# Kernel optimization log

Measured on AMD Instinct MI355X. Metric: run time of the kernel, lower is better.

Reference implementation:

```python
import jax, jax.numpy as jnp
import numpy as np

B, D, P, K, L_S = 512, 1024, 64, 16, 16


def _make_M():
    # fixed signed mask: top-left PxP block = -1, bottom-left KxP block = +1
    M = np.zeros((P + K, P + K), dtype=np.float32)
    M[:P, :P] = -1.0
    M[P:, :P] = +1.0
    return jnp.asarray(M)


def setup_inputs() -> dict:
    key = jax.random.key(0)
    k1, k2, k3 = jax.random.split(key, 3)
    X_tilde = jax.random.normal(k1, (B, D, P + K), dtype=jnp.float32)
    y_train = jax.random.normal(k2, (B, P), dtype=jnp.float32)
    gamma = jax.random.normal(k3, (D,), dtype=jnp.float32) * 0.01
    return {"X_tilde": X_tilde, "y_train": y_train, "gamma": gamma}


def reference(X_tilde, y_train, gamma):
    M = _make_M()  # [P+K, P+K]
    Bsz = X_tilde.shape[0]
    # h0 = [y_train, 0_K]  -> [B, P+K]
    h0 = jnp.concatenate([y_train, jnp.zeros((Bsz, K), dtype=y_train.dtype)], axis=-1)
    # score[b,m,n] = sum_d gamma[d] * X[b,d,m] * X[b,d,n] / P
    weighted = gamma[None, :, None] * X_tilde  # [B, D, P+K]
    score = jnp.einsum('bdm,bdn->bmn', weighted, X_tilde) / float(P)
    masked_score = M[None, :, :] * score  # [B, P+K, P+K]
    inv_L = 1.0 / float(L_S)

    def step(h, _):
        h = h + inv_L * jnp.einsum('bmn,bn->bm', masked_score, h)
        return h, None

    h, _ = jax.lax.scan(step, h0, None, length=L_S)
    return h[:, P:]
```

## Files before the change

### kernel.cpp

```cpp
#include <hip/hip_runtime.h>


namespace {
typedef __attribute__((ext_vector_type(8))) short bf16x8;
typedef __attribute__((ext_vector_type(4))) float f32x4;
typedef __attribute__((ext_vector_type(4))) float fv4;
typedef __attribute__((ext_vector_type(2))) unsigned uv2;

constexpr int kB  = 512;
constexpr int kD  = 1024;
constexpr int kP  = 64;
constexpr int kKK = 16;
constexpr int kLS = 16;
constexpr int kThreads = 640;
constexpr int kKc = 64;
constexpr int kNC = kD / kKc;

constexpr int TB    = 4096;
constexpr int ASZ   = 80 * 64 * 2;
constexpr int BSZ   = 64 * 64 * 2;
constexpr int BUFSZ = ASZ + BSZ;
constexpr int LDS_BYTES = TB + 2 * BUFSZ;

__device__ __forceinline__ unsigned short bf16_bits(float x) {
  unsigned u = __builtin_bit_cast(unsigned, x);
  u += 0x7fffu + ((u >> 16) & 1u);
  return (unsigned short)(u >> 16);
}
__device__ __forceinline__ unsigned bpack(float lo, float hi) {
  return (unsigned)bf16_bits(lo) | ((unsigned)bf16_bits(hi) << 16);
}

__global__ void __launch_bounds__(kThreads)
tcsf_kernel(const float* __restrict__ X, const float* __restrict__ y,
            const float* __restrict__ gamma, float* __restrict__ out) {
  __shared__ __align__(16) char smem[LDS_BYTES];
  float* gs = reinterpret_cast<float*>(smem);

  const int t = threadIdx.x;
  const int b = blockIdx.x;
  const int l = t & 63;
  const int w = t >> 6;
  const int grp = (w >= 5) ? 1 : 0;
  const int slab = grp ? (w - 5) : w;
  const int tg = grp ? (t - 320) : t;
  const int ct = tg % 20;
  const int kt = tg / 20;

  for (int i = t; i < kD; i += kThreads) gs[i] = gamma[i];

  const fv4* Xg = reinterpret_cast<const fv4*>(X) + (size_t)b * (kD * 80 / 4);

  f32x4 acc[4];
#pragma unroll
  for (int nt = 0; nt < 4; ++nt) acc[nt] = (f32x4)(0.f);

  fv4 v0, v1, v2, v3;

  const int rA   = 16 * slab + (l & 15);
  const int cb   = grp * 64 + (l >> 4) * 16;
  const int fswz = (l & 7) << 4;

  {
    const int c0 = grp;
    const int base = (c0 * kKc + 4 * kt) * 20 + ct;
    v0 = Xg[base]; v1 = Xg[base + 20]; v2 = Xg[base + 40]; v3 = Xg[base + 60];
  }
  __syncthreads();
  if (grp == 0) {
    char* Ab = smem + TB;
    char* Bb = Ab + ASZ;
    const fv4 g4 = *reinterpret_cast<const fv4*>(gs + 4 * kt);
#pragma unroll
    for (int j = 0; j < 4; ++j) {
      const int m = 4 * ct + j;
      const int rowo = m * 128;
      const int col = (8 * kt) ^ ((m & 7) << 4);
      uv2 wa; wa.x = bpack(v0[j], v1[j]); wa.y = bpack(v2[j], v3[j]);
      *reinterpret_cast<uv2*>(Ab + rowo + col) = wa;
      if (ct < 16) {
        uv2 wb; wb.x = bpack(g4[0] * v0[j], g4[1] * v1[j]);
        wb.y = bpack(g4[2] * v2[j], g4[3] * v3[j]);
        *reinterpret_cast<uv2*>(Bb + rowo + col) = wb;
      }
    }
  }
  __syncthreads();

  for (int c = 0; c < kNC; ++c) {
    const int pl = c & 1;
    if (c + 2 < kNC && grp == pl) {
      const int base = ((c + 2) * kKc + 4 * kt) * 20 + ct;
      v0 = Xg[base]; v1 = Xg[base + 20]; v2 = Xg[base + 40]; v3 = Xg[base + 60];
    }
    if (c + 1 < kNC && grp != pl) {
      char* Ab = smem + TB + ((c + 1) & 1) * BUFSZ;
      char* Bb = Ab + ASZ;
      const fv4 g4 = *reinterpret_cast<const fv4*>(gs + (c + 1) * kKc + 4 * kt);
#pragma unroll
      for (int j = 0; j < 4; ++j) {
        const int m = 4 * ct + j;
        const int rowo = m * 128;
        const int col = (8 * kt) ^ ((m & 7) << 4);
        uv2 wa; wa.x = bpack(v0[j], v1[j]); wa.y = bpack(v2[j], v3[j]);
        *reinterpret_cast<uv2*>(Ab + rowo + col) = wa;
        if (ct < 16) {
          uv2 wb; wb.x = bpack(g4[0] * v0[j], g4[1] * v1[j]);
          wb.y = bpack(g4[2] * v2[j], g4[3] * v3[j]);
          *reinterpret_cast<uv2*>(Bb + rowo + col) = wb;
        }
      }
    }
    {
      const char* Ab = smem + TB + pl * BUFSZ;
      const char* Bb = Ab + ASZ;
      const bf16x8 a = *reinterpret_cast<const bf16x8*>(Ab + rA * 128 + (cb ^ fswz));
#pragma unroll
      for (int nt = 0; nt < 4; ++nt) {
        const bf16x8 bb = *reinterpret_cast<const bf16x8*>(
            Bb + (16 * nt + (l & 15)) * 128 + (cb ^ fswz));
        acc[nt] = __builtin_amdgcn_mfma_f32_16x16x32_bf16(a, bb, acc[nt], 0, 0, 0);
      }
    }
    __syncthreads();
  }

  float* Gl = reinterpret_cast<float*>(smem + TB);
  float* hp = Gl + 80 * 65;
  constexpr float invP = 1.0f / 64.0f;
  if (grp) {
#pragma unroll
    for (int nt = 0; nt < 4; ++nt)
#pragma unroll
      for (int r = 0; r < 4; ++r)
        Gl[(16 * slab + (l >> 4) * 4 + r) * 65 + 16 * nt + (l & 15)] = acc[nt][r];
  }
  __syncthreads();
  if (!grp) {
#pragma unroll
    for (int nt = 0; nt < 4; ++nt)
#pragma unroll
      for (int r = 0; r < 4; ++r) {
        const int idx = (16 * slab + (l >> 4) * 4 + r) * 65 + 16 * nt + (l & 15);
        Gl[idx] = (Gl[idx] + acc[nt][r]) * invP;
      }
  }
  if (t < kP) hp[t] = y[b * kP + t];
  __syncthreads();

  const int m = t >> 3;
  const int part = t & 7;
  const float* Grow = Gl + m * 65 + part * 8;
  float hk = 0.f;
  constexpr float invL = 1.0f / kLS;
  for (int s = 0; s < kLS; ++s) {
    const float* hpc = hp + (s & 1) * kP;
    const float* hpp = hpc + part * 8;
    float d0 = 0.f, d1 = 0.f, d2 = 0.f, d3 = 0.f;
#pragma unroll
    for (int i = 0; i < 8; i += 4) {
      d0 = fmaf(Grow[i + 0], hpp[i + 0], d0);
      d1 = fmaf(Grow[i + 1], hpp[i + 1], d1);
      d2 = fmaf(Grow[i + 2], hpp[i + 2], d2);
      d3 = fmaf(Grow[i + 3], hpp[i + 3], d3);
    }
    float dot = (d0 + d1) + (d2 + d3);
    dot += __shfl_xor(dot, 1);
    dot += __shfl_xor(dot, 2);
    dot += __shfl_xor(dot, 4);
    if (part == 0) {
      if (m < kP) hp[((s + 1) & 1) * kP + m] = hpc[m] - invL * dot;
      else        hk += invL * dot;
    }
    __syncthreads();
  }
  if (part == 0 && m >= kP) out[b * kKK + (m - kP)] = hk;
}

}

extern "C" void kernel_launch(void* const* d_in, const int* in_sizes, int n_in,
                              void* d_out, int out_size, void* d_ws, size_t ws_size,
                              hipStream_t stream) {
  const float* X     = (const float*)d_in[0];
  const float* y     = (const float*)d_in[1];
  const float* gamma = (const float*)d_in[2];
  float* out = (float*)d_out;
  tcsf_kernel<<<dim3(kB), dim3(kThreads), 0, stream>>>(X, y, gamma, out);
}
```

Baseline: 41.30 us.

## Reorder prefetch after staging, change LDS swizzle, hoist offsets and y load

Each group now stages its register-held chunk into LDS first and then issues the global loads for chunk c+3, rather than loading before staging. This makes the loaded registers free earlier and gives the loads a full iteration to arrive. The XOR swizzle now also mixes row bits 2-4 to cut LDS bank conflicts between writes and reads. MFMA fragment offsets are hoisted out of the loop, and the y load is issued at kernel start to hide its latency. The cost is a slightly more complex swizzle computation.

```diff
diff --git a/kernel.cpp b/kernel.cpp
--- a/kernel.cpp
+++ b/kernel.cpp
@@ -17,8 +17,8 @@
 constexpr int kNC = kD / kKc;
 
 constexpr int TB    = 4096;
-constexpr int ASZ   = 80 * 64 * 2;
-constexpr int BSZ   = 64 * 64 * 2;
+constexpr int ASZ   = 80 * 128;
+constexpr int BSZ   = 64 * 128;
 constexpr int BUFSZ = ASZ + BSZ;
 constexpr int LDS_BYTES = TB + 2 * BUFSZ;
 
@@ -29,6 +29,28 @@
 }
 __device__ __forceinline__ unsigned bpack(float lo, float hi) {
   return (unsigned)bf16_bits(lo) | ((unsigned)bf16_bits(hi) << 16);
+}
+__device__ __forceinline__ int fswz(int r) {
+  return ((r & 7) ^ ((r >> 2) & 7)) << 4;
+}
+
+__device__ __forceinline__ void stage_chunk(char* __restrict__ Ab, char* __restrict__ Bb,
+                                            int ct, int kt,
+                                            const fv4& v0, const fv4& v1,
+                                            const fv4& v2, const fv4& v3,
+                                            const fv4& g4) {
+#pragma unroll
+  for (int j = 0; j < 4; ++j) {
+    const int m = 4 * ct + j;
+    const int off = m * 128 + ((8 * kt) ^ fswz(m));
+    uv2 wa; wa.x = bpack(v0[j], v1[j]); wa.y = bpack(v2[j], v3[j]);
+    *reinterpret_cast<uv2*>(Ab + off) = wa;
+    if (ct < 16) {
+      uv2 wb; wb.x = bpack(g4[0] * v0[j], g4[1] * v1[j]);
+      wb.y = bpack(g4[2] * v2[j], g4[3] * v3[j]);
+      *reinterpret_cast<uv2*>(Bb + off) = wb;
+    }
+  }
 }
 
 __global__ void __launch_bounds__(kThreads)
@@ -47,6 +69,8 @@
   const int ct = tg % 20;
   const int kt = tg / 20;
 
+  float yv = 0.f;
+  if (t < kP) yv = y[b * kP + t];
   for (int i = t; i < kD; i += kThreads) gs[i] = gamma[i];
 
   const fv4* Xg = reinterpret_cast<const fv4*>(X) + (size_t)b * (kD * 80 / 4);
@@ -57,70 +81,48 @@
 
   fv4 v0, v1, v2, v3;
 
-  const int rA   = 16 * slab + (l & 15);
-  const int cb   = grp * 64 + (l >> 4) * 16;
-  const int fswz = (l & 7) << 4;
-
   {
-    const int c0 = grp;
-    const int base = (c0 * kKc + 4 * kt) * 20 + ct;
+    const int base = (grp * kKc + 4 * kt) * 20 + ct;
     v0 = Xg[base]; v1 = Xg[base + 20]; v2 = Xg[base + 40]; v3 = Xg[base + 60];
   }
   __syncthreads();
-  if (grp == 0) {
-    char* Ab = smem + TB;
-    char* Bb = Ab + ASZ;
+  if (!grp) {
     const fv4 g4 = *reinterpret_cast<const fv4*>(gs + 4 * kt);
-#pragma unroll
-    for (int j = 0; j < 4; ++j) {
-      const int m = 4 * ct + j;
-      const int rowo = m * 128;
-      const int col = (8 * kt) ^ ((m & 7) << 4);
-      uv2 wa; wa.x = bpack(v0[j], v1[j]); wa.y = bpack(v2[j], v3[j]);
-      *reinterpret_cast<uv2*>(Ab + rowo + col) = wa;
-      if (ct < 16) {
-        uv2 wb; wb.x = bpack(g4[0] * v0[j], g4[1] * v1[j]);
-        wb.y = bpack(g4[2] * v2[j], g4[3] * v3[j]);
-        *reinterpret_cast<uv2*>(Bb + rowo + col) = wb;
-      }
-    }
+    stage_chunk(smem + TB, smem + TB + ASZ, ct, kt, v0, v1, v2, v3, g4);
+    const int base = (2 * kKc + 4 * kt) * 20 + ct;
+    v0 = Xg[base]; v1 = Xg[base + 20]; v2 = Xg[base + 40]; v3 = Xg[base + 60];
   }
   __syncthreads();
 
+  const int rA = 16 * slab + (l & 15);
+  const int cbb = grp * 64 + (l >> 4) * 16;
+  const int offA = rA * 128 + (cbb ^ fswz(rA));
+  int offB[4];
+#pragma unroll
+  for (int nt = 0; nt < 4; ++nt) {
+    const int rB = 16 * nt + (l & 15);
+    offB[nt] = rB * 128 + (cbb ^ fswz(rB));
+  }
+
   for (int c = 0; c < kNC; ++c) {
-    const int pl = c & 1;
-    if (c + 2 < kNC && grp == pl) {
-      const int base = ((c + 2) * kKc + 4 * kt) * 20 + ct;
-      v0 = Xg[base]; v1 = Xg[base + 20]; v2 = Xg[base + 40]; v3 = Xg[base + 60];
-    }
-    if (c + 1 < kNC && grp != pl) {
-      char* Ab = smem + TB + ((c + 1) & 1) * BUFSZ;
-      char* Bb = Ab + ASZ;
-      const fv4 g4 = *reinterpret_cast<const fv4*>(gs + (c + 1) * kKc + 4 * kt);
-#pragma unroll
-      for (int j = 0; j < 4; ++j) {
-        const int m = 4 * ct + j;
-        const int rowo = m * 128;
-        const int col = (8 * kt) ^ ((m & 7) << 4);
-        uv2 wa; wa.x = bpack(v0[j], v1[j]); wa.y = bpack(v2[j], v3[j]);
-        *reinterpret_cast<uv2*>(Ab + rowo + col) = wa;
-        if (ct < 16) {
-          uv2 wb; wb.x = bpack(g4[0] * v0[j], g4[1] * v1[j]);
-          wb.y = bpack(g4[2] * v2[j], g4[3] * v3[j]);
-          *reinterpret_cast<uv2*>(Bb + rowo + col) = wb;
-        }
+    if (grp == ((c + 1) & 1)) {
+      if (c + 1 < kNC) {
+        const fv4 g4 = *reinterpret_cast<const fv4*>(gs + (c + 1) * kKc + 4 * kt);
+        char* Ab = smem + TB + ((c + 1) & 1) * BUFSZ;
+        stage_chunk(Ab, Ab + ASZ, ct, kt, v0, v1, v2, v3, g4);
+      }
+      if (c + 3 < kNC) {
+        const int base = ((c + 3) * kKc + 4 * kt) * 20 + ct;
+        v0 = Xg[base]; v1 = Xg[base + 20]; v2 = Xg[base + 40]; v3 = Xg[base + 60];
       }
     }
-    {
-      const char* Ab = smem + TB + pl * BUFSZ;
-      const char* Bb = Ab + ASZ;
-      const bf16x8 a = *reinterpret_cast<const bf16x8*>(Ab + rA * 128 + (cb ^ fswz));
+    const char* Ab = smem + TB + (c & 1) * BUFSZ;
+    const char* Bb = Ab + ASZ;
+    const bf16x8 a = *reinterpret_cast<const bf16x8*>(Ab + offA);
 #pragma unroll
-      for (int nt = 0; nt < 4; ++nt) {
-        const bf16x8 bb = *reinterpret_cast<const bf16x8*>(
-            Bb + (16 * nt + (l & 15)) * 128 + (cb ^ fswz));
-        acc[nt] = __builtin_amdgcn_mfma_f32_16x16x32_bf16(a, bb, acc[nt], 0, 0, 0);
-      }
+    for (int nt = 0; nt < 4; ++nt) {
+      const bf16x8 bb = *reinterpret_cast<const bf16x8*>(Bb + offB[nt]);
+      acc[nt] = __builtin_amdgcn_mfma_f32_16x16x32_bf16(a, bb, acc[nt], 0, 0, 0);
     }
     __syncthreads();
   }
@@ -145,7 +147,7 @@
         Gl[idx] = (Gl[idx] + acc[nt][r]) * invP;
       }
   }
-  if (t < kP) hp[t] = y[b * kP + t];
+  if (t < kP) hp[t] = yv;
   __syncthreads();
 
   const int m = t >> 3;
```

After: 41.06 us. Within noise of the previous version (-0.6%).
